# Kernel optimization log

Hardware: AMD Instinct MI355X
Metric: run time of the kernel (lower is better)

## Reference

```python
import jax, jax.numpy as jnp
import numpy as np

B, N, D, H = 4, 2048, 1024, 8
HD = D // H  # head_dim = 128
TEMPER = 1.0
LN_EPS = 1e-5


def setup_inputs() -> dict:
    key = jax.random.key(0)
    ks = jax.random.split(key, 6)
    return {
        "h": jax.random.normal(ks[0], (B, N, D), dtype=jnp.float32),
        "Wl": jax.random.normal(ks[1], (D, D), dtype=jnp.float32) * (D ** -0.5),
        "Wr": jax.random.normal(ks[2], (D, D), dtype=jnp.float32) * (D ** -0.5),
        "att_l": jax.random.normal(ks[3], (1, HD), dtype=jnp.float32) * (HD ** -0.5),
        "att_r": jax.random.normal(ks[4], (1, HD), dtype=jnp.float32) * (HD ** -0.5),
        "Wf": jax.random.normal(ks[5], (D, D), dtype=jnp.float32) * (D ** -0.5),
        "ln_gamma": jnp.ones((D,), dtype=jnp.float32),
        "ln_beta": jnp.zeros((D,), dtype=jnp.float32),
    }


def _leaky(x):
    return jnp.where(x > 0, x, 0.01 * x)


def reference(h, Wl, Wr, att_l, att_r, Wf, ln_gamma, ln_beta):
    b, n, d = h.shape
    # projections -> [B, H, N, HD]
    fl = (h @ Wl.T).reshape(b, n, H, HD).transpose(0, 2, 1, 3)
    fr = (h @ Wr.T).reshape(b, n, H, HD).transpose(0, 2, 1, 3)
    # additive (GAT-style) scores: sl[b,h,i] + sr[b,h,j]
    sl = jnp.einsum("bhnd,d->bhn", _leaky(fl), att_l[0])
    sr = jnp.einsum("bhnd,d->bhn", _leaky(fr), att_r[0])
    score = (sl[:, :, :, None] + sr[:, :, None, :]) / TEMPER  # [B,H,N,N]
    p = jax.nn.softmax(score, axis=-1)
    # context and merge heads
    ctx = jnp.einsum("bhnm,bhmd->bhnd", p, fr)
    h_sa = ctx.transpose(0, 2, 1, 3).reshape(b, n, d)
    fh = h_sa @ Wf.T
    y = h + fh
    mu = jnp.mean(y, axis=-1, keepdims=True)
    var = jnp.mean(jnp.square(y - mu), axis=-1, keepdims=True)
    return (y - mu) * jax.lax.rsqrt(var + LN_EPS) * ln_gamma + ln_beta
```

## Files before the change

kernel.cpp:

```cpp
#include <hip/hip_runtime.h>
#include <hip/hip_bf16.h>

#define B_ 4
#define N_ 2048
#define D_ 1024
#define H_ 8
#define HD_ 128

typedef __attribute__((ext_vector_type(4))) float f32x4;
typedef __attribute__((ext_vector_type(8))) short bf16x8;

__device__ __forceinline__ short f2bf(float f) {
    unsigned u = __builtin_bit_cast(unsigned, f);
    u = (u + 0x7FFFu + ((u >> 16) & 1u)) >> 16;
    return (short)u;
}

typedef const __attribute__((address_space(1))) void* gas_t;
typedef __attribute__((address_space(3))) void* las_t;

__device__ __forceinline__ void gload16(const void* g, void* l) {
    __builtin_amdgcn_global_load_lds((gas_t)g, (las_t)l, 16, 0, 0);
}

__global__ __launch_bounds__(256) void k_cvt(
    const float* __restrict__ src, short* __restrict__ dst, int n8)
{
    const int i = blockIdx.x * 256 + threadIdx.x;
    if (i >= n8) return;
    float4 a = ((const float4*)src)[i * 2];
    float4 b = ((const float4*)src)[i * 2 + 1];
    bf16x8 o;
    o[0] = f2bf(a.x); o[1] = f2bf(a.y); o[2] = f2bf(a.z); o[3] = f2bf(a.w);
    o[4] = f2bf(b.x); o[5] = f2bf(b.y); o[6] = f2bf(b.z); o[7] = f2bf(b.w);
    ((bf16x8*)dst)[i] = o;
}

__global__ __launch_bounds__(256) void k_proj_sr(
    const short* __restrict__ hb, const short* __restrict__ wrb,
    const float* __restrict__ att_r, float* __restrict__ sr)
{
    __shared__ short sA[128 * 32];
    __shared__ short sB[128 * 32];
    __shared__ float part[2][128];

    const int tid  = threadIdx.x;
    const int lane = tid & 63;
    const int wave = tid >> 6;
    const int cc   = lane & 15;
    const int g    = lane >> 4;
    const int wr   = wave >> 1;
    const int wc   = wave & 1;
    const int rowBase = blockIdx.x * 128;
    const int head    = blockIdx.y;

    const int r0q0 = (wave * 2) * 16 + (lane >> 2);
    const int colb = (lane & 3) * 8;
    const short* gA0 = hb  + (size_t)(rowBase + r0q0) * D_ + colb;
    const short* gB0 = wrb + (size_t)(head * HD_ + r0q0) * D_ + colb;
    char* lA = (char*)sA + (size_t)(wave * 2) * 1024;
    char* lB = (char*)sB + (size_t)(wave * 2) * 1024;

    f32x4 acc[4][4];
#pragma unroll
    for (int m = 0; m < 4; ++m)
#pragma unroll
        for (int n = 0; n < 4; ++n) acc[m][n] = (f32x4){0.f, 0.f, 0.f, 0.f};

    for (int k0 = 0; k0 < D_; k0 += 32) {
        gload16(gA0 + k0,            lA);
        gload16(gA0 + k0 + 16 * D_,  lA + 1024);
        gload16(gB0 + k0,            lB);
        gload16(gB0 + k0 + 16 * D_,  lB + 1024);
        __syncthreads();

        bf16x8 aF[4], bF[4];
#pragma unroll
        for (int m = 0; m < 4; ++m)
            aF[m] = *(const bf16x8*)(sA + ((wr * 64 + m * 16 + cc) * 32 + g * 8));
#pragma unroll
        for (int n = 0; n < 4; ++n)
            bF[n] = *(const bf16x8*)(sB + ((wc * 64 + n * 16 + cc) * 32 + g * 8));
#pragma unroll
        for (int m = 0; m < 4; ++m)
#pragma unroll
            for (int n = 0; n < 4; ++n)
                acc[m][n] = __builtin_amdgcn_mfma_f32_16x16x32_bf16(
                    aF[m], bF[n], acc[m][n], 0, 0, 0);
        __syncthreads();
    }

    float ar[4];
#pragma unroll
    for (int n = 0; n < 4; ++n) ar[n] = att_r[wc * 64 + n * 16 + cc];

#pragma unroll
    for (int m = 0; m < 4; ++m) {
#pragma unroll
        for (int r = 0; r < 4; ++r) {
            float p = 0.f;
#pragma unroll
            for (int n = 0; n < 4; ++n) {
                float v = acc[m][n][r];
                v = v > 0.f ? v : 0.01f * v;
                p += v * ar[n];
            }
            p += __shfl_xor(p, 1); p += __shfl_xor(p, 2);
            p += __shfl_xor(p, 4); p += __shfl_xor(p, 8);
            if (cc == 0) part[wc][wr * 64 + m * 16 + g * 4 + r] = p;
        }
    }
    __syncthreads();
    if (tid < 128) {
        const int grow = rowBase + tid;
        const int b = grow >> 11, j = grow & (N_ - 1);
        sr[(size_t)(b * H_ + head) * N_ + j] = part[0][tid] + part[1][tid];
    }
}

__global__ __launch_bounds__(256) void k_softmax(
    const float* __restrict__ sr, float* __restrict__ w)
{
    const int bh = blockIdx.x;
    const int tid = threadIdx.x;
    const int lane = tid & 63, wave = tid >> 6;
    const float* s = sr + (size_t)bh * N_;
    float* o = w + (size_t)bh * N_;

    float v[8];
    float mx = -1e30f;
#pragma unroll
    for (int i = 0; i < 8; ++i) { v[i] = s[tid + i * 256]; mx = fmaxf(mx, v[i]); }
#pragma unroll
    for (int m = 1; m < 64; m <<= 1) mx = fmaxf(mx, __shfl_xor(mx, m));

    __shared__ float rmax[4], rsum[4];
    if (lane == 0) rmax[wave] = mx;
    __syncthreads();
    mx = fmaxf(fmaxf(rmax[0], rmax[1]), fmaxf(rmax[2], rmax[3]));

    float sum = 0.f;
#pragma unroll
    for (int i = 0; i < 8; ++i) { v[i] = expf(v[i] - mx); sum += v[i]; }
#pragma unroll
    for (int m = 1; m < 64; m <<= 1) sum += __shfl_xor(sum, m);
    if (lane == 0) rsum[wave] = sum;
    __syncthreads();
    sum = rsum[0] + rsum[1] + rsum[2] + rsum[3];
    const float inv = 1.f / sum;
#pragma unroll
    for (int i = 0; i < 8; ++i) o[tid + i * 256] = v[i] * inv;
}

__global__ __launch_bounds__(256) void k_hbar_partial(
    const float* __restrict__ h, const float* __restrict__ w,
    float* __restrict__ hp)
{
    const int dc = blockIdx.x;
    const int jc = blockIdx.y;
    const int b  = blockIdx.z;
    const int tid = threadIdx.x;
    const int d = dc * 256 + tid;

    __shared__ float wl[8][256];
#pragma unroll
    for (int hh = 0; hh < 8; ++hh)
        wl[hh][tid] = w[(size_t)(b * H_ + hh) * N_ + jc * 256 + tid];
    __syncthreads();

    float acc[8] = {0.f, 0.f, 0.f, 0.f, 0.f, 0.f, 0.f, 0.f};
    const float* hp0 = h + ((size_t)(b * N_ + jc * 256)) * D_ + d;
    for (int jj = 0; jj < 256; ++jj) {
        float hv = hp0[(size_t)jj * D_];
#pragma unroll
        for (int hh = 0; hh < 8; ++hh) acc[hh] += wl[hh][jj] * hv;
    }
#pragma unroll
    for (int hh = 0; hh < 8; ++hh)
        hp[((size_t)(jc * 32) + b * 8 + hh) * D_ + d] = acc[hh];
}

__global__ __launch_bounds__(256) void k_hbar_reduce(
    const float* __restrict__ hp, float* __restrict__ hbar)
{
    const int i = blockIdx.x * 256 + threadIdx.x;
    float s = 0.f;
#pragma unroll
    for (int jc = 0; jc < 8; ++jc) s += hp[(size_t)jc * 32768 + i];
    hbar[i] = s;
}

__global__ __launch_bounds__(256) void k_ctx(
    const float* __restrict__ hbar, const float* __restrict__ Wr,
    float* __restrict__ ctx)
{
    const int o = blockIdx.x * 4 + (threadIdx.x >> 6);
    const int lane = threadIdx.x & 63;
    const int b = o >> 10, rem = o & 1023;
    const int head = rem >> 7;
    const float* x  = hbar + (size_t)(b * H_ + head) * D_;
    const float* wr = Wr + (size_t)rem * D_;
    float s = 0.f;
#pragma unroll
    for (int it = 0; it < 4; ++it) {
        float4 xv = *(const float4*)(x + it * 256 + lane * 4);
        float4 wv = *(const float4*)(wr + it * 256 + lane * 4);
        s += xv.x * wv.x + xv.y * wv.y + xv.z * wv.z + xv.w * wv.w;
    }
#pragma unroll
    for (int m = 1; m < 64; m <<= 1) s += __shfl_xor(s, m);
    if (lane == 0) ctx[o] = s;
}

__global__ __launch_bounds__(256) void k_fvec(
    const float* __restrict__ ctx, const float* __restrict__ Wf,
    float* __restrict__ fvec)
{
    const int o = blockIdx.x * 4 + (threadIdx.x >> 6);
    const int lane = threadIdx.x & 63;
    const int b = o >> 10, orow = o & 1023;
    const float* x  = ctx + (size_t)b * D_;
    const float* wf = Wf + (size_t)orow * D_;
    float s = 0.f;
#pragma unroll
    for (int it = 0; it < 4; ++it) {
        float4 xv = *(const float4*)(x + it * 256 + lane * 4);
        float4 wv = *(const float4*)(wf + it * 256 + lane * 4);
        s += xv.x * wv.x + xv.y * wv.y + xv.z * wv.z + xv.w * wv.w;
    }
#pragma unroll
    for (int m = 1; m < 64; m <<= 1) s += __shfl_xor(s, m);
    if (lane == 0) fvec[o] = s;
}

__global__ __launch_bounds__(256) void k_ln(
    const float* __restrict__ h, const float* __restrict__ fvec,
    const float* __restrict__ gamma, const float* __restrict__ beta,
    float* __restrict__ out)
{
    const int row = blockIdx.x;
    const int b = row >> 11;
    const int tid = threadIdx.x;
    const int lane = tid & 63, wave = tid >> 6;

    float4 hv = *(const float4*)(h + (size_t)row * D_ + tid * 4);
    float4 fv = *(const float4*)(fvec + (size_t)b * D_ + tid * 4);
    const float y0 = hv.x + fv.x, y1 = hv.y + fv.y;
    const float y2 = hv.z + fv.z, y3 = hv.w + fv.w;

    float s = y0 + y1 + y2 + y3;
    float q = y0 * y0 + y1 * y1 + y2 * y2 + y3 * y3;
#pragma unroll
    for (int m = 1; m < 64; m <<= 1) { s += __shfl_xor(s, m); q += __shfl_xor(q, m); }

    __shared__ float rs[4], rq[4];
    if (lane == 0) { rs[wave] = s; rq[wave] = q; }
    __syncthreads();
    s = rs[0] + rs[1] + rs[2] + rs[3];
    q = rq[0] + rq[1] + rq[2] + rq[3];

    const float mu  = s * (1.f / D_);
    const float var = q * (1.f / D_) - mu * mu;
    const float inv = rsqrtf(var + 1e-5f);

    float4 gv = *(const float4*)(gamma + tid * 4);
    float4 bv = *(const float4*)(beta + tid * 4);
    float4 ov;
    ov.x = (y0 - mu) * inv * gv.x + bv.x;
    ov.y = (y1 - mu) * inv * gv.y + bv.y;
    ov.z = (y2 - mu) * inv * gv.z + bv.z;
    ov.w = (y3 - mu) * inv * gv.w + bv.w;
    *(float4*)(out + (size_t)row * D_ + tid * 4) = ov;
}

extern "C" void kernel_launch(void* const* d_in, const int* in_sizes, int n_in,
                              void* d_out, int out_size, void* d_ws, size_t ws_size,
                              hipStream_t stream) {
    const float* h     = (const float*)d_in[0];
    const float* Wr    = (const float*)d_in[2];
    const float* att_r = (const float*)d_in[4];
    const float* Wf    = (const float*)d_in[5];
    const float* gamma = (const float*)d_in[6];
    const float* beta  = (const float*)d_in[7];
    float* out = (float*)d_out;

    short* hb  = (short*)d_out;
    short* wrb = (short*)((char*)d_out + 16 * 1024 * 1024);

    char* ws = (char*)d_ws;
    float* sr   = (float*)(ws);
    float* w    = (float*)(ws + 262144);
    float* hp   = (float*)(ws + 524288);
    float* hbar = (float*)(ws + 1572864);
    float* ctx  = (float*)(ws + 1703936);
    float* fvec = (float*)(ws + 1720320);

    k_cvt<<<4096, 256, 0, stream>>>(h,  hb,  (B_ * N_ * D_) / 8);
    k_cvt<<<512,  256, 0, stream>>>(Wr, wrb, (D_ * D_) / 8);
    k_proj_sr<<<dim3((B_ * N_) / 128, H_), 256, 0, stream>>>(hb, wrb, att_r, sr);
    k_softmax<<<B_ * H_, 256, 0, stream>>>(sr, w);
    k_hbar_partial<<<dim3(4, 8, 4), 256, 0, stream>>>(h, w, hp);
    k_hbar_reduce<<<128, 256, 0, stream>>>(hp, hbar);
    k_ctx<<<1024, 256, 0, stream>>>(hbar, Wr, ctx);
    k_fvec<<<1024, 256, 0, stream>>>(ctx, Wf, fvec);
    k_ln<<<B_ * N_, 256, 0, stream>>>(h, fvec, gamma, beta, out);
}
```

Before: 79.68 us.

## Merge conversion launches, widen GEMM K-tile, read bf16 h, fuse hbar reduce into ctx

Folds the two fp32-to-bf16 conversion launches into one grid and widens the projection GEMM K-step from 32 to 64 with a swizzled workgroup-to-tile mapping. The hbar partial kernel now reads the bf16 copy of h instead of fp32, halving that traffic at some precision cost. The separate hbar reduction kernel is removed; the ctx kernel sums the partials into shared memory itself and computes all 128 outputs per (batch, head) block. These cut launch count and memory traffic, but the ctx kernel now runs on only 32 blocks, which limits parallelism.

```diff
diff --git a/kernel.cpp b/kernel.cpp
--- a/kernel.cpp
+++ b/kernel.cpp
@@ -15,6 +15,10 @@
     u = (u + 0x7FFFu + ((u >> 16) & 1u)) >> 16;
     return (short)u;
 }
+__device__ __forceinline__ float bf2f(unsigned short s) {
+    unsigned u = (unsigned)s << 16;
+    return __builtin_bit_cast(float, u);
+}
 
 typedef const __attribute__((address_space(1))) void* gas_t;
 typedef __attribute__((address_space(3))) void* las_t;
@@ -24,10 +28,15 @@
 }
 
 __global__ __launch_bounds__(256) void k_cvt(
-    const float* __restrict__ src, short* __restrict__ dst, int n8)
-{
-    const int i = blockIdx.x * 256 + threadIdx.x;
-    if (i >= n8) return;
+    const float* __restrict__ h, short* __restrict__ hb,
+    const float* __restrict__ Wr, short* __restrict__ wrb)
+{
+    int blk = blockIdx.x;
+    const float* src;
+    short* dst;
+    int i;
+    if (blk < 4096) { src = h;  dst = hb;  i = blk * 256 + threadIdx.x; }
+    else            { src = Wr; dst = wrb; i = (blk - 4096) * 256 + threadIdx.x; }
     float4 a = ((const float4*)src)[i * 2];
     float4 b = ((const float4*)src)[i * 2 + 1];
     bf16x8 o;
@@ -40,8 +49,8 @@
     const short* __restrict__ hb, const short* __restrict__ wrb,
     const float* __restrict__ att_r, float* __restrict__ sr)
 {
-    __shared__ short sA[128 * 32];
-    __shared__ short sB[128 * 32];
+    __shared__ short sA[128 * 64];
+    __shared__ short sB[128 * 64];
     __shared__ float part[2][128];
 
     const int tid  = threadIdx.x;
@@ -51,15 +60,18 @@
     const int g    = lane >> 4;
     const int wr   = wave >> 1;
     const int wc   = wave & 1;
-    const int rowBase = blockIdx.x * 128;
-    const int head    = blockIdx.y;
-
-    const int r0q0 = (wave * 2) * 16 + (lane >> 2);
-    const int colb = (lane & 3) * 8;
-    const short* gA0 = hb  + (size_t)(rowBase + r0q0) * D_ + colb;
-    const short* gB0 = wrb + (size_t)(head * HD_ + r0q0) * D_ + colb;
-    char* lA = (char*)sA + (size_t)(wave * 2) * 1024;
-    char* lB = (char*)sB + (size_t)(wave * 2) * 1024;
+
+    const int wg   = blockIdx.x;
+    const int swz  = (wg & 7) * 64 + (wg >> 3);
+    const int rowBase = (swz & 63) * 128;
+    const int head    = swz >> 6;
+
+    const int srow = lane >> 3;
+    const int scol = (lane & 7) * 8;
+    const short* gA0 = hb  + (size_t)(rowBase + wave * 32 + srow) * D_ + scol;
+    const short* gB0 = wrb + (size_t)(head * HD_ + wave * 32 + srow) * D_ + scol;
+    char* lA = (char*)sA + wave * 32 * 128;
+    char* lB = (char*)sB + wave * 32 * 128;
 
     f32x4 acc[4][4];
 #pragma unroll
@@ -67,26 +79,31 @@
 #pragma unroll
         for (int n = 0; n < 4; ++n) acc[m][n] = (f32x4){0.f, 0.f, 0.f, 0.f};
 
-    for (int k0 = 0; k0 < D_; k0 += 32) {
-        gload16(gA0 + k0,            lA);
-        gload16(gA0 + k0 + 16 * D_,  lA + 1024);
-        gload16(gB0 + k0,            lB);
-        gload16(gB0 + k0 + 16 * D_,  lB + 1024);
+    for (int k0 = 0; k0 < D_; k0 += 64) {
+#pragma unroll
+        for (int q = 0; q < 4; ++q)
+            gload16(gA0 + k0 + q * 8 * D_, lA + q * 1024);
+#pragma unroll
+        for (int q = 0; q < 4; ++q)
+            gload16(gB0 + k0 + q * 8 * D_, lB + q * 1024);
         __syncthreads();
 
-        bf16x8 aF[4], bF[4];
-#pragma unroll
-        for (int m = 0; m < 4; ++m)
-            aF[m] = *(const bf16x8*)(sA + ((wr * 64 + m * 16 + cc) * 32 + g * 8));
-#pragma unroll
-        for (int n = 0; n < 4; ++n)
-            bF[n] = *(const bf16x8*)(sB + ((wc * 64 + n * 16 + cc) * 32 + g * 8));
-#pragma unroll
-        for (int m = 0; m < 4; ++m)
+#pragma unroll
+        for (int kk = 0; kk < 2; ++kk) {
+            bf16x8 aF[4], bF[4];
+#pragma unroll
+            for (int m = 0; m < 4; ++m)
+                aF[m] = *(const bf16x8*)(sA + (wr * 64 + m * 16 + cc) * 64 + kk * 32 + g * 8);
 #pragma unroll
             for (int n = 0; n < 4; ++n)
-                acc[m][n] = __builtin_amdgcn_mfma_f32_16x16x32_bf16(
-                    aF[m], bF[n], acc[m][n], 0, 0, 0);
+                bF[n] = *(const bf16x8*)(sB + (wc * 64 + n * 16 + cc) * 64 + kk * 32 + g * 8);
+#pragma unroll
+            for (int m = 0; m < 4; ++m)
+#pragma unroll
+                for (int n = 0; n < 4; ++n)
+                    acc[m][n] = __builtin_amdgcn_mfma_f32_16x16x32_bf16(
+                        aF[m], bF[n], acc[m][n], 0, 0, 0);
+        }
         __syncthreads();
     }
 
@@ -153,7 +170,7 @@
 }
 
 __global__ __launch_bounds__(256) void k_hbar_partial(
-    const float* __restrict__ h, const float* __restrict__ w,
+    const short* __restrict__ hbm, const float* __restrict__ w,
     float* __restrict__ hp)
 {
     const int dc = blockIdx.x;
@@ -169,9 +186,9 @@
     __syncthreads();
 
     float acc[8] = {0.f, 0.f, 0.f, 0.f, 0.f, 0.f, 0.f, 0.f};
-    const float* hp0 = h + ((size_t)(b * N_ + jc * 256)) * D_ + d;
+    const short* hp0 = hbm + ((size_t)(b * N_ + jc * 256)) * D_ + d;
     for (int jj = 0; jj < 256; ++jj) {
-        float hv = hp0[(size_t)jj * D_];
+        float hv = bf2f((unsigned short)hp0[(size_t)jj * D_]);
 #pragma unroll
         for (int hh = 0; hh < 8; ++hh) acc[hh] += wl[hh][jj] * hv;
     }
@@ -180,36 +197,40 @@
         hp[((size_t)(jc * 32) + b * 8 + hh) * D_ + d] = acc[hh];
 }
 
-__global__ __launch_bounds__(256) void k_hbar_reduce(
-    const float* __restrict__ hp, float* __restrict__ hbar)
-{
-    const int i = blockIdx.x * 256 + threadIdx.x;
-    float s = 0.f;
-#pragma unroll
-    for (int jc = 0; jc < 8; ++jc) s += hp[(size_t)jc * 32768 + i];
-    hbar[i] = s;
-}
-
 __global__ __launch_bounds__(256) void k_ctx(
-    const float* __restrict__ hbar, const float* __restrict__ Wr,
+    const float* __restrict__ hp, const float* __restrict__ Wr,
     float* __restrict__ ctx)
 {
-    const int o = blockIdx.x * 4 + (threadIdx.x >> 6);
-    const int lane = threadIdx.x & 63;
-    const int b = o >> 10, rem = o & 1023;
-    const int head = rem >> 7;
-    const float* x  = hbar + (size_t)(b * H_ + head) * D_;
-    const float* wr = Wr + (size_t)rem * D_;
-    float s = 0.f;
-#pragma unroll
-    for (int it = 0; it < 4; ++it) {
-        float4 xv = *(const float4*)(x + it * 256 + lane * 4);
-        float4 wv = *(const float4*)(wr + it * 256 + lane * 4);
-        s += xv.x * wv.x + xv.y * wv.y + xv.z * wv.z + xv.w * wv.w;
-    }
-#pragma unroll
-    for (int m = 1; m < 64; m <<= 1) s += __shfl_xor(s, m);
-    if (lane == 0) ctx[o] = s;
+    const int bh = blockIdx.x;
+    const int b = bh >> 3, head = bh & 7;
+    const int tid = threadIdx.x;
+    const int lane = tid & 63, wave = tid >> 6;
+
+    __shared__ float xs[1024];
+    float4 s = {0.f, 0.f, 0.f, 0.f};
+#pragma unroll
+    for (int jc = 0; jc < 8; ++jc) {
+        float4 v = ((const float4*)(hp + ((size_t)(jc * 32) + bh) * D_))[tid];
+        s.x += v.x; s.y += v.y; s.z += v.z; s.w += v.w;
+    }
+    ((float4*)xs)[tid] = s;
+    __syncthreads();
+
+#pragma unroll
+    for (int oo = 0; oo < 32; ++oo) {
+        const int o = wave * 32 + oo;
+        const float* wrow = Wr + (size_t)(head * HD_ + o) * D_;
+        float acc = 0.f;
+#pragma unroll
+        for (int it = 0; it < 4; ++it) {
+            float4 wv = *(const float4*)(wrow + it * 256 + lane * 4);
+            float4 xv = ((const float4*)xs)[it * 64 + lane];
+            acc += wv.x * xv.x + wv.y * xv.y + wv.z * xv.z + wv.w * xv.w;
+        }
+#pragma unroll
+        for (int m = 1; m < 64; m <<= 1) acc += __shfl_xor(acc, m);
+        if (lane == 0) ctx[(size_t)b * D_ + head * HD_ + o] = acc;
+    }
 }
 
 __global__ __launch_bounds__(256) void k_fvec(
@@ -291,17 +312,14 @@
     float* sr   = (float*)(ws);
     float* w    = (float*)(ws + 262144);
     float* hp   = (float*)(ws + 524288);
-    float* hbar = (float*)(ws + 1572864);
-    float* ctx  = (float*)(ws + 1703936);
-    float* fvec = (float*)(ws + 1720320);
-
-    k_cvt<<<4096, 256, 0, stream>>>(h,  hb,  (B_ * N_ * D_) / 8);
-    k_cvt<<<512,  256, 0, stream>>>(Wr, wrb, (D_ * D_) / 8);
-    k_proj_sr<<<dim3((B_ * N_) / 128, H_), 256, 0, stream>>>(hb, wrb, att_r, sr);
+    float* ctx  = (float*)(ws + 1572864);
+    float* fvec = (float*)(ws + 1589248);
+
+    k_cvt<<<4096 + 512, 256, 0, stream>>>(h, hb, Wr, wrb);
+    k_proj_sr<<<(B_ * N_ / 128) * H_, 256, 0, stream>>>(hb, wrb, att_r, sr);
     k_softmax<<<B_ * H_, 256, 0, stream>>>(sr, w);
-    k_hbar_partial<<<dim3(4, 8, 4), 256, 0, stream>>>(h, w, hp);
-    k_hbar_reduce<<<128, 256, 0, stream>>>(hp, hbar);
-    k_ctx<<<1024, 256, 0, stream>>>(hbar, Wr, ctx);
+    k_hbar_partial<<<dim3(4, 8, 4), 256, 0, stream>>>(hb, w, hp);
+    k_ctx<<<B_ * H_, 256, 0, stream>>>(hp, Wr, ctx);
     k_fvec<<<1024, 256, 0, stream>>>(ctx, Wf, fvec);
     k_ln<<<B_ * N_, 256, 0, stream>>>(h, fvec, gamma, beta, out);
 }
```

After: 99.00 us. 24.2% more time.
